# Performance work log

Measured on AMD Instinct MI355X. Metric: run time of the kernel, lower is better.

Reference implementation:

```python
import jax, jax.numpy as jnp
import numpy as np

I = 256   # input_size
H = 256   # hidden_size
B = 64
T = 2048


def setup_inputs() -> dict:
    key = jax.random.key(0)
    ks = jax.random.split(key, 7)
    s_i = 1.0 / np.sqrt(I)
    s_h = 1.0 / np.sqrt(H)
    return {
        "x": jax.random.normal(ks[0], (B, T, I), dtype=jnp.float32),
        "h0": jax.random.normal(ks[1], (1, B, H), dtype=jnp.float32),
        "c0": jax.random.normal(ks[2], (1, B, H), dtype=jnp.float32),
        # Only l_fi / l_fh affect the output in the original forward (all four
        # gates are computed from the same pre-activation due to a source bug).
        "W_fi": jax.random.uniform(ks[3], (H, I), jnp.float32, -s_i, s_i),
        "b_fi": jax.random.uniform(ks[4], (H,), jnp.float32, -s_i, s_i),
        "W_fh": jax.random.uniform(ks[5], (H, H), jnp.float32, -s_h, s_h),
        "b_fh": jax.random.uniform(ks[6], (H,), jnp.float32, -s_h, s_h),
    }


def reference(x, h0, c0, W_fi, b_fi, W_fh, b_fh):
    # Faithful to the buggy torch source:
    #   f = i = o = sigmoid(l_fi(x_t) + l_fh(ht_1)); m = tanh(same)
    #   ht_1, ct_1 are NEVER updated -> no recurrence; vectorize over time.
    ht_1 = h0[0]  # (B, H), state[0].squeeze(0)
    ct_1 = c0[0]  # (B, H)
    gx = jnp.einsum('bti,hi->bth', x, W_fi) + b_fi          # (B, T, H)
    gh = ht_1 @ W_fh.T + b_fh                               # (B, H)
    g = gx + gh[:, None, :]                                 # (B, T, H)
    s = jax.nn.sigmoid(g)
    m = jnp.tanh(g)
    c = s * ct_1[:, None, :] + s * m                        # c_t per step
    h = s * jnp.tanh(c)                                     # h_t per step
    hidden_seq = jnp.transpose(h, (1, 0, 2))                # (T, B, H), cat dim=0
    return (hidden_seq, (h[:, -1, :], c[:, -1, :]))
```

## Files before the change

kernel.cpp:

```cpp
#include <hip/hip_runtime.h>
#include <hip/hip_bf16.h>
#include <stdint.h>

#define T_SZ 2048
#define B_SZ 64
#define H_SZ 256
#define I_SZ 256
#define M_SZ (B_SZ * T_SZ)
#define TBH  (T_SZ * B_SZ * H_SZ)

typedef float f32x4 __attribute__((ext_vector_type(4)));
typedef short s16x8 __attribute__((ext_vector_type(8)));

__device__ __forceinline__ unsigned pack_bf16(float a, float b) {
    unsigned ua = __float_as_uint(a);
    unsigned ub = __float_as_uint(b);
    ua += 0x7fffu + ((ua >> 16) & 1u);
    ub += 0x7fffu + ((ub >> 16) & 1u);
    return (ua >> 16) | (ub & 0xffff0000u);
}

__device__ __forceinline__ void gload_lds16(const unsigned short* g, unsigned short* l) {
    __builtin_amdgcn_global_load_lds(
        (const __attribute__((address_space(1))) unsigned int*)g,
        (__attribute__((address_space(3))) unsigned int*)l,
        16, 0, 0);
}

__global__ void prep_kernel(const float* __restrict__ h0,
                            const float* __restrict__ W_fi,
                            const float* __restrict__ b_fi,
                            const float* __restrict__ W_fh,
                            const float* __restrict__ b_fh,
                            unsigned short* __restrict__ Wb,
                            float* __restrict__ gb) {
    __shared__ float h0s[H_SZ];
    const int b = blockIdx.x;
    const int h = threadIdx.x;
    h0s[h] = h0[b * H_SZ + h];
    __syncthreads();
    const float4* w4 = (const float4*)(W_fh + (size_t)h * H_SZ);
    float acc = 0.f;
#pragma unroll 8
    for (int j = 0; j < H_SZ / 4; ++j) {
        float4 w = w4[j];
        acc = fmaf(w.x, h0s[4 * j + 0], acc);
        acc = fmaf(w.y, h0s[4 * j + 1], acc);
        acc = fmaf(w.z, h0s[4 * j + 2], acc);
        acc = fmaf(w.w, h0s[4 * j + 3], acc);
    }
    gb[b * H_SZ + h] = acc + b_fi[h] + b_fh[h];

    const int e = (b * 256 + h) * 4;
    float4 wv = *(const float4*)(W_fi + e);
    uint2 pk;
    pk.x = pack_bf16(wv.x, wv.y);
    pk.y = pack_bf16(wv.z, wv.w);
    *(uint2*)(Wb + e) = pk;
}

__global__ __launch_bounds__(256) void lstm_main(
    const float* __restrict__ x,
    const unsigned short* __restrict__ Wb,
    const float* __restrict__ gb,
    const float* __restrict__ c0,
    float* __restrict__ out) {
    __shared__ __align__(16) unsigned short As[128 * 32];
    __shared__ __align__(16) unsigned short Bs[128 * 32];

    const int tid  = threadIdx.x;
    const int lane = tid & 63;
    const int wid  = tid >> 6;
    const int bid  = blockIdx.x;
    const int mt = bid >> 1, nt = bid & 1;
    const int m0 = mt * 128, n0 = nt * 128;
    const int wm = (wid & 1) * 64, wn = (wid >> 1) * 64;

    f32x4 acc[4][4];
#pragma unroll
    for (int mi = 0; mi < 4; ++mi)
#pragma unroll
        for (int ni = 0; ni < 4; ++ni)
            acc[mi][ni] = (f32x4){0.f, 0.f, 0.f, 0.f};

    const int am = tid >> 2, aq = tid & 3;
    const float* aptr0 = x + (size_t)(m0 + am) * I_SZ + aq * 8;
    const float* aptr1 = aptr0 + (size_t)64 * I_SZ;

    const int bslot0 = wid * 64 + lane;
    const int bslot1 = 256 + bslot0;
    const int br0 = bslot0 >> 2, bq0 = bslot0 & 3;
    const int br1 = bslot1 >> 2, bq1 = bslot1 & 3;
    const unsigned short* bsrc0 = Wb + (size_t)(n0 + br0) * I_SZ + bq0 * 8;
    const unsigned short* bsrc1 = Wb + (size_t)(n0 + br1) * I_SZ + bq1 * 8;
    unsigned short* bdst0 = Bs + (size_t)(wid * 64) * 8;
    unsigned short* bdst1 = Bs + (size_t)(256 + wid * 64) * 8;

    const int fr = lane & 15;
    const int fq = lane >> 4;

    for (int kt = 0; kt < 8; ++kt) {
        const int kof = kt * 32;
        if (kt) __syncthreads();

        const float4* p0 = (const float4*)(aptr0 + kof);
        const float4* p1 = (const float4*)(aptr1 + kof);
        float4 v0 = p0[0], v1 = p0[1];
        float4 v2 = p1[0], v3 = p1[1];

        gload_lds16(bsrc0 + kof, bdst0);
        gload_lds16(bsrc1 + kof, bdst1);

        uint4 pa, pb;
        pa.x = pack_bf16(v0.x, v0.y); pa.y = pack_bf16(v0.z, v0.w);
        pa.z = pack_bf16(v1.x, v1.y); pa.w = pack_bf16(v1.z, v1.w);
        pb.x = pack_bf16(v2.x, v2.y); pb.y = pack_bf16(v2.z, v2.w);
        pb.z = pack_bf16(v3.x, v3.y); pb.w = pack_bf16(v3.z, v3.w);
        *(uint4*)(As + (size_t)tid * 8) = pa;
        *(uint4*)(As + (size_t)(256 + tid) * 8) = pb;

        __syncthreads();

        s16x8 af[4], bf[4];
#pragma unroll
        for (int mi = 0; mi < 4; ++mi)
            af[mi] = *(const s16x8*)(As + (wm + mi * 16 + fr) * 32 + fq * 8);
#pragma unroll
        for (int ni = 0; ni < 4; ++ni)
            bf[ni] = *(const s16x8*)(Bs + (wn + ni * 16 + fr) * 32 + fq * 8);
#pragma unroll
        for (int mi = 0; mi < 4; ++mi)
#pragma unroll
            for (int ni = 0; ni < 4; ++ni)
                acc[mi][ni] = __builtin_amdgcn_mfma_f32_16x16x32_bf16(
                    af[mi], bf[ni], acc[mi][ni], 0, 0, 0);
    }

    const int coln = n0 + wn + fr;
#pragma unroll
    for (int mi = 0; mi < 4; ++mi) {
#pragma unroll
        for (int r = 0; r < 4; ++r) {
            const int Mg = m0 + wm + mi * 16 + fq * 4 + r;
            const int bb = Mg >> 11;
            const int tt = Mg & (T_SZ - 1);
            const int obase = tt * (B_SZ * H_SZ) + bb * H_SZ;
            const float* gbrow = gb + bb * H_SZ;
            const float* c0row = c0 + bb * H_SZ;
            const bool last = (tt == T_SZ - 1);
#pragma unroll
            for (int ni = 0; ni < 4; ++ni) {
                const int h = coln + ni * 16;
                float g = acc[mi][ni][r] + gbrow[h];
                float gc = fminf(15.f, fmaxf(-15.f, g));
                float e = __expf(-gc);
                float s = __builtin_amdgcn_rcpf(1.f + e);
                float e2 = e * e;
                float m = (1.f - e2) * __builtin_amdgcn_rcpf(1.f + e2);
                float cv = s * (c0row[h] + m);
                float cc = fminf(15.f, fmaxf(-15.f, cv));
                float ec = __expf(-2.f * cc);
                float th = (1.f - ec) * __builtin_amdgcn_rcpf(1.f + ec);
                float hv = s * th;
                out[obase + h] = hv;
                if (last) {
                    out[TBH + bb * H_SZ + h] = hv;
                    out[TBH + B_SZ * H_SZ + bb * H_SZ + h] = cv;
                }
            }
        }
    }
}

extern "C" void kernel_launch(void* const* d_in, const int* in_sizes, int n_in,
                              void* d_out, int out_size, void* d_ws, size_t ws_size,
                              hipStream_t stream) {
    const float* x    = (const float*)d_in[0];
    const float* h0   = (const float*)d_in[1];
    const float* c0   = (const float*)d_in[2];
    const float* W_fi = (const float*)d_in[3];
    const float* b_fi = (const float*)d_in[4];
    const float* W_fh = (const float*)d_in[5];
    const float* b_fh = (const float*)d_in[6];
    float* out = (float*)d_out;

    unsigned short* Wb = (unsigned short*)d_ws;
    float* gb = (float*)((char*)d_ws + 131072);

    hipLaunchKernelGGL(prep_kernel, dim3(B_SZ), dim3(H_SZ), 0, stream,
                       h0, W_fi, b_fi, W_fh, b_fh, Wb, gb);
    hipLaunchKernelGGL(lstm_main, dim3(M_SZ / 128 * 2), dim3(256), 0, stream,
                       x, Wb, gb, c0, out);
}
```

Baseline: 276.9 us.

## Load x fragments directly to registers and keep full W tile in swizzled LDS

The main kernel is restructured. Each block now covers 128 rows by 64 columns with the whole 64x256 bf16 weight slab loaded once into XOR-swizzled LDS. The A operand is read from global memory straight into registers in MFMA fragment layout, with the next k-step prefetched, so the per-k-step LDS staging and barriers go away. Output stores become nontemporal, the clamps before exp are removed, and launch bounds ask for higher occupancy. The trade-off is that each x row is now read by four blocks instead of two, and the uncoalesced fragment loads may cost more global bandwidth.

```diff
diff --git a/kernel.cpp b/kernel.cpp
--- a/kernel.cpp
+++ b/kernel.cpp
@@ -18,6 +18,15 @@
     ua += 0x7fffu + ((ua >> 16) & 1u);
     ub += 0x7fffu + ((ub >> 16) & 1u);
     return (ua >> 16) | (ub & 0xffff0000u);
+}
+
+__device__ __forceinline__ s16x8 pack8(float4 lo, float4 hi) {
+    union { uint4 u; s16x8 v; } cv;
+    cv.u.x = pack_bf16(lo.x, lo.y);
+    cv.u.y = pack_bf16(lo.z, lo.w);
+    cv.u.z = pack_bf16(hi.x, hi.y);
+    cv.u.w = pack_bf16(hi.z, hi.w);
+    return cv.v;
 }
 
 __device__ __forceinline__ void gload_lds16(const unsigned short* g, unsigned short* l) {
@@ -41,7 +50,7 @@
     __syncthreads();
     const float4* w4 = (const float4*)(W_fh + (size_t)h * H_SZ);
     float acc = 0.f;
-#pragma unroll 8
+#pragma unroll 16
     for (int j = 0; j < H_SZ / 4; ++j) {
         float4 w = w4[j];
         acc = fmaf(w.x, h0s[4 * j + 0], acc);
@@ -59,110 +68,100 @@
     *(uint2*)(Wb + e) = pk;
 }
 
-__global__ __launch_bounds__(256) void lstm_main(
+__global__ __launch_bounds__(256, 4) void lstm_main(
     const float* __restrict__ x,
     const unsigned short* __restrict__ Wb,
     const float* __restrict__ gb,
     const float* __restrict__ c0,
     float* __restrict__ out) {
-    __shared__ __align__(16) unsigned short As[128 * 32];
-    __shared__ __align__(16) unsigned short Bs[128 * 32];
+    __shared__ __align__(16) unsigned short Bs[64 * 256];
 
     const int tid  = threadIdx.x;
     const int lane = tid & 63;
     const int wid  = tid >> 6;
     const int bid  = blockIdx.x;
-    const int mt = bid >> 1, nt = bid & 1;
-    const int m0 = mt * 128, n0 = nt * 128;
-    const int wm = (wid & 1) * 64, wn = (wid >> 1) * 64;
+    const int n0 = (bid & 3) * 64;
+    const int m0 = (bid >> 2) * 128;
 
-    f32x4 acc[4][4];
 #pragma unroll
-    for (int mi = 0; mi < 4; ++mi)
+    for (int i = 0; i < 8; ++i) {
+        const int cbase = wid * 512 + i * 64;
+        const int c = cbase + lane;
+        const int row = c >> 5;
+        const int kc = (lane & 31) ^ (row & 7);
+        gload_lds16(Wb + (((size_t)(n0 + row)) << 8) + (kc << 3),
+                    Bs + (size_t)cbase * 8);
+    }
+
+    const int fr = lane & 15, fq = lane >> 4;
+
+    f32x4 acc[2][4];
+#pragma unroll
+    for (int mi = 0; mi < 2; ++mi)
 #pragma unroll
         for (int ni = 0; ni < 4; ++ni)
             acc[mi][ni] = (f32x4){0.f, 0.f, 0.f, 0.f};
 
-    const int am = tid >> 2, aq = tid & 3;
-    const float* aptr0 = x + (size_t)(m0 + am) * I_SZ + aq * 8;
-    const float* aptr1 = aptr0 + (size_t)64 * I_SZ;
+    const float* a0 = x + (size_t)(m0 + wid * 32 + fr) * I_SZ + fq * 8;
+    const float* a1 = a0 + 16 * I_SZ;
 
-    const int bslot0 = wid * 64 + lane;
-    const int bslot1 = 256 + bslot0;
-    const int br0 = bslot0 >> 2, bq0 = bslot0 & 3;
-    const int br1 = bslot1 >> 2, bq1 = bslot1 & 3;
-    const unsigned short* bsrc0 = Wb + (size_t)(n0 + br0) * I_SZ + bq0 * 8;
-    const unsigned short* bsrc1 = Wb + (size_t)(n0 + br1) * I_SZ + bq1 * 8;
-    unsigned short* bdst0 = Bs + (size_t)(wid * 64) * 8;
-    unsigned short* bdst1 = Bs + (size_t)(256 + wid * 64) * 8;
+    float4 p00 = *(const float4*)a0;
+    float4 p01 = *(const float4*)(a0 + 4);
+    float4 p10 = *(const float4*)a1;
+    float4 p11 = *(const float4*)(a1 + 4);
 
-    const int fr = lane & 15;
-    const int fq = lane >> 4;
+    __syncthreads();
 
+#pragma unroll
     for (int kt = 0; kt < 8; ++kt) {
-        const int kof = kt * 32;
-        if (kt) __syncthreads();
-
-        const float4* p0 = (const float4*)(aptr0 + kof);
-        const float4* p1 = (const float4*)(aptr1 + kof);
-        float4 v0 = p0[0], v1 = p0[1];
-        float4 v2 = p1[0], v3 = p1[1];
-
-        gload_lds16(bsrc0 + kof, bdst0);
-        gload_lds16(bsrc1 + kof, bdst1);
-
-        uint4 pa, pb;
-        pa.x = pack_bf16(v0.x, v0.y); pa.y = pack_bf16(v0.z, v0.w);
-        pa.z = pack_bf16(v1.x, v1.y); pa.w = pack_bf16(v1.z, v1.w);
-        pb.x = pack_bf16(v2.x, v2.y); pb.y = pack_bf16(v2.z, v2.w);
-        pb.z = pack_bf16(v3.x, v3.y); pb.w = pack_bf16(v3.z, v3.w);
-        *(uint4*)(As + (size_t)tid * 8) = pa;
-        *(uint4*)(As + (size_t)(256 + tid) * 8) = pb;
-
-        __syncthreads();
-
-        s16x8 af[4], bf[4];
+        s16x8 af0 = pack8(p00, p01);
+        s16x8 af1 = pack8(p10, p11);
+        if (kt < 7) {
+            const int ko = (kt + 1) * 32;
+            p00 = *(const float4*)(a0 + ko);
+            p01 = *(const float4*)(a0 + ko + 4);
+            p10 = *(const float4*)(a1 + ko);
+            p11 = *(const float4*)(a1 + ko + 4);
+        }
+        s16x8 bf[4];
 #pragma unroll
-        for (int mi = 0; mi < 4; ++mi)
-            af[mi] = *(const s16x8*)(As + (wm + mi * 16 + fr) * 32 + fq * 8);
+        for (int ni = 0; ni < 4; ++ni) {
+            const int nl = ni * 16 + fr;
+            const int p = (kt * 4 + fq) ^ (nl & 7);
+            bf[ni] = *(const s16x8*)(Bs + nl * 256 + p * 8);
+        }
 #pragma unroll
-        for (int ni = 0; ni < 4; ++ni)
-            bf[ni] = *(const s16x8*)(Bs + (wn + ni * 16 + fr) * 32 + fq * 8);
-#pragma unroll
-        for (int mi = 0; mi < 4; ++mi)
-#pragma unroll
-            for (int ni = 0; ni < 4; ++ni)
-                acc[mi][ni] = __builtin_amdgcn_mfma_f32_16x16x32_bf16(
-                    af[mi], bf[ni], acc[mi][ni], 0, 0, 0);
+        for (int ni = 0; ni < 4; ++ni) {
+            acc[0][ni] = __builtin_amdgcn_mfma_f32_16x16x32_bf16(af0, bf[ni], acc[0][ni], 0, 0, 0);
+            acc[1][ni] = __builtin_amdgcn_mfma_f32_16x16x32_bf16(af1, bf[ni], acc[1][ni], 0, 0, 0);
+        }
     }
 
-    const int coln = n0 + wn + fr;
+    const int hbase = n0 + fr;
 #pragma unroll
-    for (int mi = 0; mi < 4; ++mi) {
+    for (int mi = 0; mi < 2; ++mi) {
 #pragma unroll
         for (int r = 0; r < 4; ++r) {
-            const int Mg = m0 + wm + mi * 16 + fq * 4 + r;
+            const int Mg = m0 + wid * 32 + mi * 16 + fq * 4 + r;
             const int bb = Mg >> 11;
             const int tt = Mg & (T_SZ - 1);
-            const int obase = tt * (B_SZ * H_SZ) + bb * H_SZ;
+            float* orow = out + (size_t)tt * (B_SZ * H_SZ) + bb * H_SZ;
             const float* gbrow = gb + bb * H_SZ;
             const float* c0row = c0 + bb * H_SZ;
             const bool last = (tt == T_SZ - 1);
 #pragma unroll
             for (int ni = 0; ni < 4; ++ni) {
-                const int h = coln + ni * 16;
+                const int h = hbase + ni * 16;
                 float g = acc[mi][ni][r] + gbrow[h];
-                float gc = fminf(15.f, fmaxf(-15.f, g));
-                float e = __expf(-gc);
+                float e = __expf(-g);
                 float s = __builtin_amdgcn_rcpf(1.f + e);
                 float e2 = e * e;
                 float m = (1.f - e2) * __builtin_amdgcn_rcpf(1.f + e2);
                 float cv = s * (c0row[h] + m);
-                float cc = fminf(15.f, fmaxf(-15.f, cv));
-                float ec = __expf(-2.f * cc);
+                float ec = __expf(-2.f * cv);
                 float th = (1.f - ec) * __builtin_amdgcn_rcpf(1.f + ec);
                 float hv = s * th;
-                out[obase + h] = hv;
+                __builtin_nontemporal_store(hv, orow + h);
                 if (last) {
                     out[TBH + bb * H_SZ + h] = hv;
                     out[TBH + B_SZ * H_SZ + bb * H_SZ + h] = cv;
@@ -189,6 +188,6 @@
 
     hipLaunchKernelGGL(prep_kernel, dim3(B_SZ), dim3(H_SZ), 0, stream,
                        h0, W_fi, b_fi, W_fh, b_fh, Wb, gb);
-    hipLaunchKernelGGL(lstm_main, dim3(M_SZ / 128 * 2), dim3(256), 0, stream,
+    hipLaunchKernelGGL(lstm_main, dim3(M_SZ / 128 * 4), dim3(256), 0, stream,
                        x, Wb, gb, c0, out);
 }
```

After: 303.7 us. 1.1x slower.
